# Kernel optimization log

Hardware: AMD Instinct MI355X
Metric: run time of the kernel (lower is better)

## Reference

```python
import jax, jax.numpy as jnp
import numpy as np

Z, N, D_MODEL, HEADS = 2, 2048, 1024, 16
DK = D_MODEL // HEADS


def setup_inputs() -> dict:
    key = jax.random.key(0)
    ks = jax.random.split(key, 9)
    xavier = (6.0 / (DK + D_MODEL)) ** 0.5
    x = jax.random.normal(ks[0], (Z, N, D_MODEL), jnp.float32)
    mask = jax.random.randint(ks[1], (Z, N), 0, 2) > 0  # bool validity mask
    q_proj = jax.random.uniform(ks[2], (HEADS, D_MODEL, DK), jnp.float32, -xavier, xavier)
    k_proj = jax.random.uniform(ks[3], (HEADS, D_MODEL, DK), jnp.float32, -xavier, xavier)
    v_proj = jax.random.uniform(ks[4], (HEADS, D_MODEL, DK), jnp.float32, -xavier, xavier)
    q_bias = jnp.zeros((HEADS, DK), jnp.float32)
    k_bias = jnp.zeros((HEADS, DK), jnp.float32)
    v_bias = jnp.zeros((HEADS, DK), jnp.float32)
    lim = 1.0 / (D_MODEL ** 0.5)
    out_w = jax.random.uniform(ks[5], (D_MODEL, D_MODEL), jnp.float32, -lim, lim)  # torch Linear weight [out, in]
    return {"x": x, "mask": mask, "q_proj": q_proj, "k_proj": k_proj, "v_proj": v_proj,
            "q_bias": q_bias, "k_bias": k_bias, "v_bias": v_bias, "out_w": out_w}


def reference(x, mask, q_proj, k_proj, v_proj, q_bias, k_bias, v_bias, out_w):
    # Per-head QKV projections: [Z,N,Dm] x [H,Dm,Dk] -> [Z,H,N,Dk]
    Q = jnp.einsum('znd,hdk->zhnk', x, q_proj) + q_bias[None, :, None, :]
    K = jnp.einsum('znd,hdk->zhnk', x, k_proj) + k_bias[None, :, None, :]
    V = jnp.einsum('znd,hdk->zhnk', x, v_proj) + v_bias[None, :, None, :]
    scale = q_proj.shape[-1] ** -0.5
    # Dense equivalent of flash_attn_varlen over valid (unpadded) tokens:
    # mask invalid keys, softmax, then zero outputs at invalid query positions.
    scores = jnp.einsum('zhnk,zhmk->zhnm', Q, K) * scale
    neg = jnp.asarray(-1e9, scores.dtype)
    scores = jnp.where(mask[:, None, None, :], scores, neg)
    attn = jax.nn.softmax(scores, axis=-1)
    ctx = jnp.einsum('zhnm,zhmk->zhnk', attn, V)
    ctx = jnp.where(mask[:, None, :, None], ctx, jnp.zeros((), ctx.dtype))
    z, h, n, dk = ctx.shape
    out = ctx.transpose(0, 2, 1, 3).reshape(z, n, h * dk)  # [Z,N,Dm]
    return out @ out_w.T  # nn.Linear(d_model, d_model, bias=False)
```

## Files before the change

kernel.cpp:

```cpp
#include <hip/hip_runtime.h>
#include <stdint.h>

typedef __bf16 bf16_t;
typedef __bf16 bf16x8 __attribute__((ext_vector_type(8)));
typedef __bf16 bf16x4 __attribute__((ext_vector_type(4)));
typedef float f32x4 __attribute__((ext_vector_type(4)));

#define MFMA16(A, B, C) __builtin_amdgcn_mfma_f32_16x16x32_bf16(A, B, C, 0, 0, 0)

#if __has_builtin(__builtin_amdgcn_exp2f)
#define EXP2F(x) __builtin_amdgcn_exp2f(x)
#else
#define EXP2F(x) exp2f(x)
#endif

#define GLOAD_LDS16(g, l)                                                   \
  __builtin_amdgcn_global_load_lds(                                         \
      (const __attribute__((address_space(1))) void*)(g),                   \
      (__attribute__((address_space(3))) void*)(l), 16, 0, 0)

#define SL2E 0.18033688011112042f
#define VT_STRIDE 131072

__global__ __launch_bounds__(256) void convert_kernel(
    const float* __restrict__ x, const float* __restrict__ qw, const float* __restrict__ kw,
    const float* __restrict__ vw, const float* __restrict__ qb, const float* __restrict__ kb,
    const float* __restrict__ vb, const float* __restrict__ ow,
    bf16_t* __restrict__ xb, bf16_t* __restrict__ wqkv, bf16_t* __restrict__ wo,
    float* __restrict__ bias)
{
  const int bid = blockIdx.x, tid = threadIdx.x;
  if (bid < 768) {
    __shared__ float tile[64][65];
    int sh = bid >> 4, db = bid & 15;
    int sec = sh >> 4, h = sh & 15;
    int d0 = db * 64;
    const float* w = sec == 0 ? qw : (sec == 1 ? kw : vw);
    int dd = tid >> 2, kk0 = (tid & 3) * 16;
    const float* src = &w[((int64_t)h * 1024 + d0 + dd) * 64 + kk0];
#pragma unroll
    for (int j = 0; j < 4; j++) {
      float4 v = *(const float4*)&src[j * 4];
      tile[dd][kk0 + j * 4 + 0] = v.x;
      tile[dd][kk0 + j * 4 + 1] = v.y;
      tile[dd][kk0 + j * 4 + 2] = v.z;
      tile[dd][kk0 + j * 4 + 3] = v.w;
    }
    __syncthreads();
    int kk = tid >> 2, dd0 = (tid & 3) * 16;
    bf16x8 o0, o1;
#pragma unroll
    for (int j = 0; j < 8; j++) o0[j] = (bf16_t)tile[dd0 + j][kk];
#pragma unroll
    for (int j = 0; j < 8; j++) o1[j] = (bf16_t)tile[dd0 + 8 + j][kk];
    bf16_t* dst = &wqkv[(int64_t)(sh * 64 + kk) * 1024 + d0 + dd0];
    *(bf16x8*)dst = o0;
    *(bf16x8*)(dst + 8) = o1;
  } else if (bid < 2816) {
    int64_t base = ((int64_t)(bid - 768) * 256 + tid) * 8;
    float4 a = *(const float4*)&x[base];
    float4 b = *(const float4*)&x[base + 4];
    bf16x8 o = {(bf16_t)a.x, (bf16_t)a.y, (bf16_t)a.z, (bf16_t)a.w,
                (bf16_t)b.x, (bf16_t)b.y, (bf16_t)b.z, (bf16_t)b.w};
    *(bf16x8*)&xb[base] = o;
  } else if (bid < 3328) {
    int64_t base = ((int64_t)(bid - 2816) * 256 + tid) * 8;
    float4 a = *(const float4*)&ow[base];
    float4 b = *(const float4*)&ow[base + 4];
    bf16x8 o = {(bf16_t)a.x, (bf16_t)a.y, (bf16_t)a.z, (bf16_t)a.w,
                (bf16_t)b.x, (bf16_t)b.y, (bf16_t)b.z, (bf16_t)b.w};
    *(bf16x8*)&wo[base] = o;
  } else {
    for (int j = tid; j < 3072; j += 256) {
      int sec = j >> 10, c = j & 1023;
      const float* b = sec == 0 ? qb : (sec == 1 ? kb : vb);
      bias[j] = b[c];
    }
  }
}

template <int MODE, int TM>
__global__ __launch_bounds__(256) void gemm_kernel(
    const bf16_t* __restrict__ A, const bf16_t* __restrict__ Bt, const float* __restrict__ bias,
    bf16_t* __restrict__ qout, bf16_t* __restrict__ kout, bf16_t* __restrict__ vtout,
    float* __restrict__ fout, int Ndim)
{
  const int Kdim = 1024;
  const int MT = TM / 32;
  const int AS_SZ = TM * 64, BS_SZ = 128 * 64, BUF = AS_SZ + BS_SZ;
  __shared__ bf16_t smem[2 * (TM * 64 + 128 * 64)];

  const int tid = threadIdx.x;
  const int wave = tid >> 6, lane = tid & 63;
  const int l15 = lane & 15, quad = lane >> 4;
  const int wr = wave >> 1, wc = wave & 1;

  const int MB = 4096 / TM;
  const int GPX = MB / 8;
  const int xcd = blockIdx.x & 7, j = blockIdx.x >> 3;
  const int bm = (xcd * GPX + (j % GPX)) * TM;
  const int bn = (j / GPX) * 128;

  f32x4 acc[MT][4] = {};

  const int lr = lane >> 3;
  const int lc = (lane & 7) * 8;

  auto stage = [&](int b, int kk) {
    bf16_t* as = smem + b * BUF;
    bf16_t* bs = as + AS_SZ;
#pragma unroll
    for (int jj = 0; jj < MT; jj++) {
      int r = wave * (TM / 4) + jj * 8;
      GLOAD_LDS16(A + (int64_t)(bm + r + lr) * Kdim + kk + lc, &as[r * 64]);
    }
#pragma unroll
    for (int jj = 0; jj < 4; jj++) {
      int r = wave * 32 + jj * 8;
      GLOAD_LDS16(Bt + (int64_t)(bn + r + lr) * Kdim + kk + lc, &bs[r * 64]);
    }
  };

  stage(0, 0);
  for (int it = 0; it < 16; ++it) {
    int cur = it & 1;
    if (it < 15) {
      asm volatile("s_waitcnt lgkmcnt(0)\n\ts_barrier" ::: "memory");
      stage(cur ^ 1, (it + 1) * 64);
      asm volatile("s_waitcnt vmcnt(%0)" ::"i"(MT + 4) : "memory");
    } else {
      asm volatile("s_waitcnt vmcnt(0)" ::: "memory");
    }
    asm volatile("s_barrier" ::: "memory");
    const bf16_t* as = smem + cur * BUF;
    const bf16_t* bs = as + AS_SZ;
#pragma unroll
    for (int kc = 0; kc < 2; kc++) {
      bf16x8 af[MT], bfr[4];
#pragma unroll
      for (int mt = 0; mt < MT; mt++)
        af[mt] = *(const bf16x8*)&as[(wr * (TM / 2) + mt * 16 + l15) * 64 + kc * 32 + quad * 8];
#pragma unroll
      for (int nt = 0; nt < 4; nt++)
        bfr[nt] = *(const bf16x8*)&bs[(wc * 64 + nt * 16 + l15) * 64 + kc * 32 + quad * 8];
#pragma unroll
      for (int mt = 0; mt < MT; mt++)
#pragma unroll
        for (int nt = 0; nt < 4; nt++) acc[mt][nt] = MFMA16(af[mt], bfr[nt], acc[mt][nt]);
    }
  }

  if (MODE == 0 && bn >= 2048) {
    __syncthreads();
    bf16_t* Ct = smem;
    const int CTS = 136;
#pragma unroll
    for (int mt = 0; mt < MT; mt++) {
#pragma unroll
      for (int nt = 0; nt < 4; nt++) {
        int c = wc * 64 + nt * 16 + l15;
        int rw = wr * (TM / 2) + mt * 16 + quad * 4;
        bf16x4 pv;
#pragma unroll
        for (int r = 0; r < 4; r++) pv[r] = (bf16_t)(acc[mt][nt][r] + bias[bn + c]);
        *(bf16x4*)&Ct[c * CTS + rw] = pv;
      }
    }
    __syncthreads();
    int z = bm >> 11, n0 = bm & 2047;
    int colb = tid >> 4, nch = (tid & 15) * 8;
#pragma unroll
    for (int p = 0; p < 8; p++) {
      int c = p * 16 + colb;
      int hk = (bn + c) & 1023;
      int hh = hk >> 6, dk = hk & 63;
      int zh = z * 16 + hh;
      bf16x8 vv = *(const bf16x8*)&Ct[c * CTS + nch];
      *(bf16x8*)&vtout[(int64_t)zh * VT_STRIDE + dk * 2048 + n0 + nch] = vv;
    }
    return;
  }

#pragma unroll
  for (int mt = 0; mt < MT; mt++) {
#pragma unroll
    for (int nt = 0; nt < 4; nt++) {
#pragma unroll
      for (int r = 0; r < 4; r++) {
        int row = bm + wr * (TM / 2) + mt * 16 + quad * 4 + r;
        int col = bn + wc * 64 + nt * 16 + l15;
        float v = acc[mt][nt][r];
        if (MODE == 0) {
          v += bias[col];
          int sec = col >> 10, hk = col & 1023;
          int hh = hk >> 6, dk = hk & 63;
          int z = row >> 11, n = row & 2047;
          int zh = z * 16 + hh;
          if (sec == 0) {
            qout[(((int64_t)zh * 2048 + n) << 6) + dk] = (bf16_t)(v * SL2E);
          } else {
            kout[(((int64_t)zh * 2048 + n) << 6) + dk] = (bf16_t)v;
          }
        } else {
          fout[(int64_t)row * Ndim + col] = v;
        }
      }
    }
  }
}

__global__ __launch_bounds__(256, 2) void attn_kernel(
    const bf16_t* __restrict__ Q, const bf16_t* __restrict__ K, const bf16_t* __restrict__ Vt,
    const int* __restrict__ mask, bf16_t* __restrict__ ctx)
{
  __shared__ bf16_t Ks[2][64 * 72];
  __shared__ bf16_t Vs[2][64 * 72];
  __shared__ float Mkf[2048];
  __shared__ bf16_t Ps[4][32 * 72];

  const int tid = threadIdx.x;
  const int wave = tid >> 6, lane = tid & 63;
  const int l15 = lane & 15, quad = lane >> 4;
  const int bid = blockIdx.x;
  const int qt = bid & 15, zh = bid >> 4;
  const int z = zh >> 4, h = zh & 15;

  const bf16_t* Qb = Q + ((int64_t)zh * 2048 + qt * 128) * 64;
  const bf16_t* Kb = K + (int64_t)zh * 2048 * 64;
  const bf16_t* Vb = Vt + (int64_t)zh * VT_STRIDE;
  bf16_t* Psw = Ps[wave];

  const int srow = lane >> 3;
  const int scol = (lane & 7) * 8;

  bf16x8 qf[2][2];
#pragma unroll
  for (int s = 0; s < 2; s++) {
    qf[s][0] = *(const bf16x8*)&Qb[(wave * 32 + s * 16 + l15) * 64 + quad * 8];
    qf[s][1] = *(const bf16x8*)&Qb[(wave * 32 + s * 16 + l15) * 64 + 32 + quad * 8];
  }

  {
    const int4* mp = (const int4*)(mask + z * 2048);
    for (int i = tid; i < 512; i += 256) {
      int4 m4 = mp[i];
      float4 f;
      f.x = m4.x ? 0.f : -1e30f;
      f.y = m4.y ? 0.f : -1e30f;
      f.z = m4.z ? 0.f : -1e30f;
      f.w = m4.w ? 0.f : -1e30f;
      *(float4*)&Mkf[i * 4] = f;
    }
  }

  {
    uint4 kp[2], vp[2];
#pragma unroll
    for (int j = 0; j < 2; j++) {
      int r = wave * 16 + j * 8 + srow;
      kp[j] = *(const uint4*)&Kb[(int64_t)r * 64 + scol];
      vp[j] = *(const uint4*)&Vb[(int64_t)r * 2048 + scol];
    }
#pragma unroll
    for (int j = 0; j < 2; j++) {
      int r = wave * 16 + j * 8 + srow;
      *(uint4*)&Ks[0][r * 72 + scol] = kp[j];
      *(uint4*)&Vs[0][r * 72 + scol] = vp[j];
    }
  }
  __syncthreads();

  float l_run[2] = {0.f, 0.f};
  f32x4 o[2][4] = {};
  int cur = 0;

  for (int kt = 0; kt < 32; kt++) {
    uint4 kp[2], vp[2];
    if (kt < 31) {
#pragma unroll
      for (int j = 0; j < 2; j++) {
        int r = wave * 16 + j * 8 + srow;
        kp[j] = *(const uint4*)&Kb[(int64_t)((kt + 1) * 64 + r) * 64 + scol];
        vp[j] = *(const uint4*)&Vb[(int64_t)r * 2048 + (kt + 1) * 64 + scol];
      }
    }

    f32x4 minit[4];
    bf16x8 kf0[4], kf1[4];
#pragma unroll
    for (int mb = 0; mb < 4; mb++) {
      minit[mb] = *(const f32x4*)&Mkf[kt * 64 + mb * 16 + quad * 4];
      kf0[mb] = *(const bf16x8*)&Ks[cur][(mb * 16 + l15) * 72 + quad * 8];
      kf1[mb] = *(const bf16x8*)&Ks[cur][(mb * 16 + l15) * 72 + 32 + quad * 8];
    }

#pragma unroll
    for (int s = 0; s < 2; s++) {
      float rs = 0.f;
#pragma unroll
      for (int mb = 0; mb < 4; mb++) {
        f32x4 t = minit[mb];
        t = MFMA16(kf0[mb], qf[s][0], t);
        t = MFMA16(kf1[mb], qf[s][1], t);
        bf16x4 pk;
#pragma unroll
        for (int r = 0; r < 4; r++) {
          float p = EXP2F(t[r]);
          rs += p;
          pk[r] = (bf16_t)p;
        }
        *(bf16x4*)&Psw[(s * 16 + l15) * 72 + mb * 16 + quad * 4] = pk;
      }
      l_run[s] += rs;
    }

    bf16x8 p0[2], p1[2];
#pragma unroll
    for (int s = 0; s < 2; s++) {
      p0[s] = *(const bf16x8*)&Psw[(s * 16 + l15) * 72 + quad * 8];
      p1[s] = *(const bf16x8*)&Psw[(s * 16 + l15) * 72 + 32 + quad * 8];
    }

#pragma unroll
    for (int nb = 0; nb < 4; nb++) {
      bf16x8 v0 = *(const bf16x8*)&Vs[cur][(nb * 16 + l15) * 72 + quad * 8];
      bf16x8 v1 = *(const bf16x8*)&Vs[cur][(nb * 16 + l15) * 72 + 32 + quad * 8];
#pragma unroll
      for (int s = 0; s < 2; s++) {
        o[s][nb] = MFMA16(p0[s], v0, o[s][nb]);
        o[s][nb] = MFMA16(p1[s], v1, o[s][nb]);
      }
    }

    if (kt < 31) {
#pragma unroll
      for (int j = 0; j < 2; j++) {
        int r = wave * 16 + j * 8 + srow;
        *(uint4*)&Ks[cur ^ 1][r * 72 + scol] = kp[j];
        *(uint4*)&Vs[cur ^ 1][r * 72 + scol] = vp[j];
      }
    }
    __syncthreads();
    cur ^= 1;
  }

#pragma unroll
  for (int s = 0; s < 2; s++) {
    float l = l_run[s];
    l += __shfl_xor(l, 16);
    l += __shfl_xor(l, 32);
    float inv4[4];
#pragma unroll
    for (int r = 0; r < 4; r++) {
      int qrow = qt * 128 + wave * 32 + s * 16 + quad * 4 + r;
      float lv = __shfl(l, quad * 4 + r);
      int valid = mask[z * 2048 + qrow];
      inv4[r] = (valid && lv > 0.f) ? 1.0f / lv : 0.f;
    }
#pragma unroll
    for (int nb = 0; nb < 4; nb++) {
#pragma unroll
      for (int r = 0; r < 4; r++) {
        int qrow = qt * 128 + wave * 32 + s * 16 + quad * 4 + r;
        ctx[((int64_t)(z * 2048 + qrow)) * 1024 + h * 64 + nb * 16 + l15] =
            (bf16_t)(o[s][nb][r] * inv4[r]);
      }
    }
  }
}

extern "C" void kernel_launch(void* const* d_in, const int* in_sizes, int n_in,
                              void* d_out, int out_size, void* d_ws, size_t ws_size,
                              hipStream_t stream)
{
  (void)in_sizes; (void)n_in; (void)out_size; (void)ws_size;
  const float* x  = (const float*)d_in[0];
  const int* mask = (const int*)d_in[1];
  const float* qw = (const float*)d_in[2];
  const float* kw = (const float*)d_in[3];
  const float* vw = (const float*)d_in[4];
  const float* qb = (const float*)d_in[5];
  const float* kb = (const float*)d_in[6];
  const float* vb = (const float*)d_in[7];
  const float* ow = (const float*)d_in[8];
  float* out = (float*)d_out;

  bf16_t* xb   = (bf16_t*)d_ws;
  bf16_t* wqkv = xb + 4194304;
  bf16_t* wo   = wqkv + 3145728;
  float*  bias = (float*)(wo + 1048576);
  bf16_t* Qb   = (bf16_t*)(bias + 3072);
  bf16_t* Kb   = Qb + 4194304;
  bf16_t* Vtb  = Kb + 4194304;
  bf16_t* ctx  = Vtb + (int64_t)32 * VT_STRIDE;

  convert_kernel<<<3329, 256, 0, stream>>>(x, qw, kw, vw, qb, kb, vb, ow,
                                           xb, wqkv, wo, bias);
  gemm_kernel<0, 128><<<(4096 / 128) * (3072 / 128), 256, 0, stream>>>(
      xb, wqkv, bias, Qb, Kb, Vtb, nullptr, 3072);
  attn_kernel<<<2 * 16 * 16, 256, 0, stream>>>(Qb, Kb, Vtb, mask, ctx);
  gemm_kernel<1, 64><<<(4096 / 64) * (1024 / 128), 256, 0, stream>>>(
      ctx, wo, nullptr, nullptr, nullptr, nullptr, out, 1024);
}
```

Measured before the change: 199.2 us.

## Read K and V fragments directly from global memory, dropping LDS staging

The attention kernel no longer stages K and V tiles through double-buffered shared memory. Each wave now loads its MFMA fragments straight from global memory, relying on L1/L2 for reuse across the four waves, and the per-iteration block barrier is removed. Launch bounds are raised to 4 blocks per CU to take advantage of the smaller LDS footprint and hide latency through occupancy. The trade-off is four times the redundant global/L2 traffic per block and exposed load latency, since there is no explicit prefetch.

```diff
diff --git a/kernel.cpp b/kernel.cpp
--- a/kernel.cpp
+++ b/kernel.cpp
@@ -209,12 +209,10 @@
   }
 }
 
-__global__ __launch_bounds__(256, 2) void attn_kernel(
+__global__ __launch_bounds__(256, 4) void attn_kernel(
     const bf16_t* __restrict__ Q, const bf16_t* __restrict__ K, const bf16_t* __restrict__ Vt,
     const int* __restrict__ mask, bf16_t* __restrict__ ctx)
 {
-  __shared__ bf16_t Ks[2][64 * 72];
-  __shared__ bf16_t Vs[2][64 * 72];
   __shared__ float Mkf[2048];
   __shared__ bf16_t Ps[4][32 * 72];
 
@@ -229,9 +227,6 @@
   const bf16_t* Kb = K + (int64_t)zh * 2048 * 64;
   const bf16_t* Vb = Vt + (int64_t)zh * VT_STRIDE;
   bf16_t* Psw = Ps[wave];
-
-  const int srow = lane >> 3;
-  const int scol = (lane & 7) * 8;
 
   bf16x8 qf[2][2];
 #pragma unroll
@@ -252,46 +247,21 @@
       *(float4*)&Mkf[i * 4] = f;
     }
   }
-
-  {
-    uint4 kp[2], vp[2];
-#pragma unroll
-    for (int j = 0; j < 2; j++) {
-      int r = wave * 16 + j * 8 + srow;
-      kp[j] = *(const uint4*)&Kb[(int64_t)r * 64 + scol];
-      vp[j] = *(const uint4*)&Vb[(int64_t)r * 2048 + scol];
-    }
-#pragma unroll
-    for (int j = 0; j < 2; j++) {
-      int r = wave * 16 + j * 8 + srow;
-      *(uint4*)&Ks[0][r * 72 + scol] = kp[j];
-      *(uint4*)&Vs[0][r * 72 + scol] = vp[j];
-    }
-  }
   __syncthreads();
 
   float l_run[2] = {0.f, 0.f};
   f32x4 o[2][4] = {};
-  int cur = 0;
 
   for (int kt = 0; kt < 32; kt++) {
-    uint4 kp[2], vp[2];
-    if (kt < 31) {
-#pragma unroll
-      for (int j = 0; j < 2; j++) {
-        int r = wave * 16 + j * 8 + srow;
-        kp[j] = *(const uint4*)&Kb[(int64_t)((kt + 1) * 64 + r) * 64 + scol];
-        vp[j] = *(const uint4*)&Vb[(int64_t)r * 2048 + (kt + 1) * 64 + scol];
-      }
-    }
+    const bf16_t* Kt = Kb + (int64_t)kt * 64 * 64;
 
     f32x4 minit[4];
     bf16x8 kf0[4], kf1[4];
 #pragma unroll
     for (int mb = 0; mb < 4; mb++) {
       minit[mb] = *(const f32x4*)&Mkf[kt * 64 + mb * 16 + quad * 4];
-      kf0[mb] = *(const bf16x8*)&Ks[cur][(mb * 16 + l15) * 72 + quad * 8];
-      kf1[mb] = *(const bf16x8*)&Ks[cur][(mb * 16 + l15) * 72 + 32 + quad * 8];
+      kf0[mb] = *(const bf16x8*)&Kt[(mb * 16 + l15) * 64 + quad * 8];
+      kf1[mb] = *(const bf16x8*)&Kt[(mb * 16 + l15) * 64 + 32 + quad * 8];
     }
 
 #pragma unroll
@@ -323,25 +293,15 @@
 
 #pragma unroll
     for (int nb = 0; nb < 4; nb++) {
-      bf16x8 v0 = *(const bf16x8*)&Vs[cur][(nb * 16 + l15) * 72 + quad * 8];
-      bf16x8 v1 = *(const bf16x8*)&Vs[cur][(nb * 16 + l15) * 72 + 32 + quad * 8];
+      const bf16_t* Vr = Vb + (int64_t)(nb * 16 + l15) * 2048 + kt * 64;
+      bf16x8 v0 = *(const bf16x8*)&Vr[quad * 8];
+      bf16x8 v1 = *(const bf16x8*)&Vr[32 + quad * 8];
 #pragma unroll
       for (int s = 0; s < 2; s++) {
         o[s][nb] = MFMA16(p0[s], v0, o[s][nb]);
         o[s][nb] = MFMA16(p1[s], v1, o[s][nb]);
       }
     }
-
-    if (kt < 31) {
-#pragma unroll
-      for (int j = 0; j < 2; j++) {
-        int r = wave * 16 + j * 8 + srow;
-        *(uint4*)&Ks[cur ^ 1][r * 72 + scol] = kp[j];
-        *(uint4*)&Vs[cur ^ 1][r * 72 + scol] = vp[j];
-      }
-    }
-    __syncthreads();
-    cur ^= 1;
   }
 
 #pragma unroll
```

After: 289.0 us. 45.1% more time.
